# Optimization experiments

Measured on AMD Instinct MI355X. Metric: run time of the kernel, lower is better.

The kernel has to match this reference:

```python
import jax, jax.numpy as jnp
import numpy as np

CH = (16, 32, 16)
T_STEPS = 30
THRESH = 1.0


def conv3d(x, w, b):
    # x: (B, Cin, D, H, W), w: (Cout, Cin, kD, kH, kW), stride 2, VALID
    y = jax.lax.conv_general_dilated(
        x, w, window_strides=(2, 2, 2), padding='VALID',
        dimension_numbers=('NCDHW', 'OIDHW', 'NCDHW'))
    return y + b[None, :, None, None, None]


def setup_inputs() -> dict:
    key = jax.random.key(0)
    ks = jax.random.split(key, 11)
    B = 4
    x = jax.random.normal(ks[0], (B, 24, 602, 602), jnp.float32)

    def uinit(k, shape, fan_in):
        bound = 1.0 / np.sqrt(fan_in)
        return jax.random.uniform(k, shape, jnp.float32, -bound, bound)

    fan1 = 1 * 3 * 15 * 15
    fan2 = CH[0] * 3 * 15 * 15
    fan3 = CH[1] * 3 * 15 * 15
    w1 = uinit(ks[1], (CH[0], 1, 3, 15, 15), fan1)
    b1 = uinit(ks[2], (CH[0],), fan1)
    w2 = uinit(ks[3], (CH[1], CH[0], 3, 15, 15), fan2)
    b2 = uinit(ks[4], (CH[1],), fan2)
    w3 = uinit(ks[5], (CH[2], CH[1], 3, 15, 15), fan3)
    b3 = uinit(ks[6], (CH[2],), fan3)
    F1 = 21632 * CH[2] // 16  # 21632 for CH[2]=16
    fc1_w = uinit(ks[7], (512, F1), F1)
    fc1_b = uinit(ks[8], (512,), F1)
    fc2_w = uinit(ks[9], (54, 512), 512)
    fc2_b = uinit(ks[10], (54,), 512)
    return dict(x=x, w1=w1, b1=b1, w2=w2, b2=b2, w3=w3, b3=b3,
                fc1_w=fc1_w, fc1_b=fc1_b, fc2_w=fc2_w, fc2_b=fc2_b)


def _forward(x, w1, b1, w2, b2, w3, b3, fc1_w, fc1_b, fc2_w, fc2_b):
    B = x.shape[0]
    # avg_pool2d(kernel=2): (B,24,602,602) -> (B,24,301,301)
    xp = x.reshape(B, 24, 301, 2, 301, 2).mean(axis=(3, 5))
    h = xp[:, None]  # (B,1,24,301,301)
    h = jax.nn.relu(conv3d(h, w1, b1))  # (B,16,11,144,144)
    h = jax.nn.relu(conv3d(h, w2, b2))  # (B,32,5,65,65)
    h = jax.nn.relu(conv3d(h, w3, b3))  # (B,16,2,26,26)
    x_snn = h.reshape(B, -1)            # (B, 21632)

    sgn = jnp.sign(x_snn)
    prob = jnp.abs(x_snn) * 0.5

    def step(carry, k):
        m0, m1 = carry
        r = jax.random.uniform(k, x_snn.shape, x_snn.dtype)
        # Poisson encoding with straight-through gradient to x_snn
        spikes = (prob > r).astype(x_snn.dtype) * sgn
        p_in = jax.lax.stop_gradient(spikes - x_snn) + x_snn
        m0 = m0 + p_in @ fc1_w.T + fc1_b
        # LIF: threshold, subtract, spike with surrogate (pass-through where fired)
        fire = m0 > THRESH
        ex = jnp.where(fire, m0, 0.0)
        m0 = m0 - ex
        out = jnp.where(fire, ex - jax.lax.stop_gradient(ex) + 1.0, 0.0)
        m1 = m1 + out @ fc2_w.T + fc2_b
        return (m0, m1), None

    keys = jax.random.split(jax.random.key(42), T_STEPS)
    init = (jnp.zeros((B, 512), x_snn.dtype), jnp.zeros((B, 54), x_snn.dtype))
    (_, m1), _ = jax.lax.scan(step, init, keys)
    return m1


def reference(x, w1, b1, w2, b2, w3, b3, fc1_w, fc1_b, fc2_w, fc2_b):
    return _forward(x, w1, b1, w2, b2, w3, b3, fc1_w, fc1_b, fc2_w, fc2_b)
```

## Files before the change

### kernel.cpp

```cpp
#include <hip/hip_runtime.h>
#include <stdint.h>

struct SnnKeys { unsigned int k0[30]; unsigned int k1[30]; };

__host__ __device__ static inline void tf2x32(unsigned int k0, unsigned int k1,
                                              unsigned int& x0, unsigned int& x1) {
  unsigned int ks2 = k0 ^ k1 ^ 0x1BD11BDAu;
#define TF_RND(r) { x0 += x1; x1 = (x1 << (r)) | (x1 >> (32 - (r))); x1 ^= x0; }
  x0 += k0; x1 += k1;
  TF_RND(13) TF_RND(15) TF_RND(26) TF_RND(6)
  x0 += k1; x1 += ks2 + 1u;
  TF_RND(17) TF_RND(29) TF_RND(16) TF_RND(24)
  x0 += ks2; x1 += k0 + 2u;
  TF_RND(13) TF_RND(15) TF_RND(26) TF_RND(6)
  x0 += k0; x1 += k1 + 3u;
  TF_RND(17) TF_RND(29) TF_RND(16) TF_RND(24)
  x0 += k1; x1 += ks2 + 4u;
  TF_RND(13) TF_RND(15) TF_RND(26) TF_RND(6)
  x0 += ks2; x1 += k0 + 5u;
#undef TF_RND
}

#define POOL_N (4 * 24 * 301 * 301)

__global__ __launch_bounds__(256) void k_pool(const float* __restrict__ x,
                                              float* __restrict__ xp) {
  int i = blockIdx.x * 256 + threadIdx.x;
  if (i >= POOL_N) return;
  int j = i % 301;
  int rest = i / 301;
  int r = rest % 301;
  int bc = rest / 301;
  const float* src = x + ((size_t)bc * 602 + 2 * r) * 602 + 2 * j;
  float2 a = *(const float2*)src;
  float2 b = *(const float2*)(src + 602);
  xp[i] = 0.25f * ((a.x + a.y) + (b.x + b.y));
}

__global__ __launch_bounds__(256) void k_wt2(const float* __restrict__ w2,
                                             float* __restrict__ w2t) {
  int i = blockIdx.x * 256 + threadIdx.x;
  if (i >= 345600) return;
  int co = i & 31;
  int rest = i >> 5;
  int ci = rest / 675;
  int k675 = rest - ci * 675;
  w2t[i] = w2[((size_t)co * 16 + ci) * 675 + k675];
}

__global__ __launch_bounds__(256) void k_wt3(const float* __restrict__ w3,
                                             float* __restrict__ w3t) {
  int i = blockIdx.x * 256 + threadIdx.x;
  if (i >= 345600) return;
  int co = i & 15;
  int rest = i >> 4;
  int ci = rest / 675;
  int k675 = rest - ci * 675;
  w3t[i] = w3[((size_t)co * 32 + ci) * 675 + k675];
}

__global__ __launch_bounds__(256) void k_conv1(const float* __restrict__ xp,
                                               const float* __restrict__ w1,
                                               const float* __restrict__ b1,
                                               float* __restrict__ h1) {
  __shared__ alignas(16) float in_e[25 * 152];
  __shared__ alignas(16) float in_o[25 * 152];
  const int tid = threadIdx.x;
  const int wave = __builtin_amdgcn_readfirstlane(tid >> 6);
  const int lane = tid & 63;
  const int cog = wave >> 1, sg = wave & 1;
  const int cob = cog * 8;
  const int bz = blockIdx.y;
  const int b = bz / 11, d = bz % 11;
  const int s0 = blockIdx.x * 512;
  const int y0 = s0 / 144;

  int sq[4], be[4];
  bool vq[4];
#pragma unroll
  for (int q = 0; q < 4; ++q) {
    int s = s0 + sg * 256 + q * 64 + lane;
    vq[q] = (s < 20736);
    int sc = vq[q] ? s : 20735;
    int y = sc / 144, xx = sc - y * 144;
    sq[q] = s;
    be[q] = 2 * (y - y0) * 152 + xx;
  }

  float acc[8][4] = {};

  for (int kd = 0; kd < 3; ++kd) {
    __syncthreads();
    const int din = 2 * d + kd;
    const float* src = xp + (size_t)(b * 24 + din) * 90601;
    for (int i = tid; i < 25 * 301; i += 256) {
      int r = i / 301, c = i - r * 301;
      int gr = 2 * y0 + r;
      float v = (gr < 301) ? src[gr * 301 + c] : 0.0f;
      ((c & 1) ? in_o : in_e)[r * 152 + (c >> 1)] = v;
    }
    __syncthreads();
    const float* wp = w1 + cob * 675 + kd * 225;
    for (int kh = 0; kh < 15; ++kh) {
      float e[4][8], o[4][7];
#pragma unroll
      for (int q = 0; q < 4; ++q) {
        const float* pe = in_e + be[q] + kh * 152;
        const float* po = in_o + be[q] + kh * 152;
#pragma unroll
        for (int j = 0; j < 8; ++j) e[q][j] = pe[j];
#pragma unroll
        for (int j = 0; j < 7; ++j) o[q][j] = po[j];
      }
      const float* wk = wp + kh * 15;
#pragma unroll
      for (int j = 0; j < 8; ++j) {
#pragma unroll
        for (int c = 0; c < 8; ++c) {
          float wv = wk[c * 675 + 2 * j];
#pragma unroll
          for (int q = 0; q < 4; ++q) acc[c][q] += wv * e[q][j];
        }
      }
#pragma unroll
      for (int j = 0; j < 7; ++j) {
#pragma unroll
        for (int c = 0; c < 8; ++c) {
          float wv = wk[c * 675 + 2 * j + 1];
#pragma unroll
          for (int q = 0; q < 4; ++q) acc[c][q] += wv * o[q][j];
        }
      }
    }
  }
#pragma unroll
  for (int q = 0; q < 4; ++q) {
    if (vq[q]) {
#pragma unroll
      for (int c = 0; c < 8; ++c) {
        float v = acc[c][q] + b1[cob + c];
        h1[((size_t)(b * 16 + cob + c) * 11 + d) * 20736 + sq[q]] = fmaxf(v, 0.0f);
      }
    }
  }
}

__global__ __launch_bounds__(256) void k_conv2(const float* __restrict__ h1,
                                               const float* __restrict__ w2t,
                                               float* __restrict__ h2p) {
  __shared__ alignas(16) float in_e[23 * 72];
  __shared__ alignas(16) float in_o[23 * 72];
  const int tid = threadIdx.x;
  const int wave = __builtin_amdgcn_readfirstlane(tid >> 6);
  const int lane = tid & 63;
  const int cob = wave * 8;
  const int bz = blockIdx.y;
  const int cig = bz & 1;
  const int t5 = bz >> 1;
  const int b = t5 / 5, d = t5 % 5;
  const int s0 = blockIdx.x * 256;
  const int y0 = s0 / 65;

  int sq[4], be[4];
  bool vq[4];
#pragma unroll
  for (int q = 0; q < 4; ++q) {
    int s = s0 + q * 64 + lane;
    vq[q] = (s < 4225);
    int sc = vq[q] ? s : 4224;
    int y = sc / 65, xx = sc - y * 65;
    sq[q] = s;
    be[q] = 2 * (y - y0) * 72 + xx;
  }

  float acc[8][4] = {};

  for (int cil = 0; cil < 8; ++cil) {
    const int ci = cig * 8 + cil;
    for (int kd = 0; kd < 3; ++kd) {
      __syncthreads();
      const int din = 2 * d + kd;
      const float* src = h1 + (size_t)((b * 16 + ci) * 11 + din) * 20736;
      for (int i = tid; i < 23 * 36; i += 256) {
        int r = i / 36, c4 = i - r * 36;
        int gr = 2 * y0 + r;
        float4 v = {0.0f, 0.0f, 0.0f, 0.0f};
        if (gr < 144) v = *(const float4*)(src + gr * 144 + c4 * 4);
        *(float2*)&in_e[r * 72 + 2 * c4] = make_float2(v.x, v.z);
        *(float2*)&in_o[r * 72 + 2 * c4] = make_float2(v.y, v.w);
      }
      __syncthreads();
      const float* wkbase = w2t + (size_t)(ci * 3 + kd) * 225 * 32 + cob;
      for (int kh = 0; kh < 15; ++kh) {
        float e[4][8], o[4][7];
#pragma unroll
        for (int q = 0; q < 4; ++q) {
          const float* pe = in_e + be[q] + kh * 72;
          const float* po = in_o + be[q] + kh * 72;
#pragma unroll
          for (int j = 0; j < 8; ++j) e[q][j] = pe[j];
#pragma unroll
          for (int j = 0; j < 7; ++j) o[q][j] = po[j];
        }
        const float* wr = wkbase + kh * 15 * 32;
#pragma unroll
        for (int j = 0; j < 8; ++j) {
#pragma unroll
          for (int c = 0; c < 8; ++c) {
            float wv = wr[(2 * j) * 32 + c];
#pragma unroll
            for (int q = 0; q < 4; ++q) acc[c][q] += wv * e[q][j];
          }
        }
#pragma unroll
        for (int j = 0; j < 7; ++j) {
#pragma unroll
          for (int c = 0; c < 8; ++c) {
            float wv = wr[(2 * j + 1) * 32 + c];
#pragma unroll
            for (int q = 0; q < 4; ++q) acc[c][q] += wv * o[q][j];
          }
        }
      }
    }
  }
#pragma unroll
  for (int q = 0; q < 4; ++q) {
    if (vq[q]) {
#pragma unroll
      for (int c = 0; c < 8; ++c) {
        h2p[(size_t)cig * 2704000 +
            ((size_t)(b * 32 + cob + c) * 5 + d) * 4225 + sq[q]] = acc[c][q];
      }
    }
  }
}

__global__ __launch_bounds__(256) void k_h2fix(const float* __restrict__ p,
                                               const float* __restrict__ b2,
                                               float* __restrict__ h2) {
  int i = blockIdx.x * 256 + threadIdx.x;
  if (i >= 2704000) return;
  int co = (i / 21125) & 31;
  float v = p[i] + p[2704000 + i] + b2[co];
  h2[i] = fmaxf(v, 0.0f);
}

__global__ __launch_bounds__(256) void k_conv3(const float* __restrict__ h2,
                                               const float* __restrict__ w3t,
                                               float* __restrict__ h3p) {
  __shared__ alignas(16) float in_e[55 * 36];
  __shared__ alignas(16) float in_o[55 * 36];
  const int tid = threadIdx.x;
  const int wave = __builtin_amdgcn_readfirstlane(tid >> 6);
  const int lane = tid & 63;
  const int cog = wave >> 1, sg = wave & 1;
  const int cob = cog * 8;
  const int bz = blockIdx.y;
  const int b = bz >> 1, d = bz & 1;
  const int cig = blockIdx.z;
  const int s0 = blockIdx.x * 512;
  const int y0 = s0 / 26;

  int sq[4], be[4];
  bool vq[4];
#pragma unroll
  for (int q = 0; q < 4; ++q) {
    int s = s0 + sg * 256 + q * 64 + lane;
    vq[q] = (s < 676);
    int sc = vq[q] ? s : 675;
    int y = sc / 26, xx = sc - y * 26;
    sq[q] = s;
    be[q] = 2 * (y - y0) * 36 + xx;
  }

  float acc[8][4] = {};

  for (int cil = 0; cil < 2; ++cil) {
    const int ci = cig * 2 + cil;
    for (int kd = 0; kd < 3; ++kd) {
      __syncthreads();
      const int din = 2 * d + kd;
      const float* src = h2 + (size_t)((b * 32 + ci) * 5 + din) * 4225;
      for (int i = tid; i < 55 * 65; i += 256) {
        int r = i / 65, c = i - r * 65;
        int gr = 2 * y0 + r;
        float v = (gr < 65) ? src[gr * 65 + c] : 0.0f;
        ((c & 1) ? in_o : in_e)[r * 36 + (c >> 1)] = v;
      }
      __syncthreads();
      const float* wkbase = w3t + (size_t)(ci * 3 + kd) * 225 * 16 + cob;
      for (int kh = 0; kh < 15; ++kh) {
        float e[4][8], o[4][7];
#pragma unroll
        for (int q = 0; q < 4; ++q) {
          const float* pe = in_e + be[q] + kh * 36;
          const float* po = in_o + be[q] + kh * 36;
#pragma unroll
          for (int j = 0; j < 8; ++j) e[q][j] = pe[j];
#pragma unroll
          for (int j = 0; j < 7; ++j) o[q][j] = po[j];
        }
        const float* wr = wkbase + kh * 15 * 16;
#pragma unroll
        for (int j = 0; j < 8; ++j) {
#pragma unroll
          for (int c = 0; c < 8; ++c) {
            float wv = wr[(2 * j) * 16 + c];
#pragma unroll
            for (int q = 0; q < 4; ++q) acc[c][q] += wv * e[q][j];
          }
        }
#pragma unroll
        for (int j = 0; j < 7; ++j) {
#pragma unroll
          for (int c = 0; c < 8; ++c) {
            float wv = wr[(2 * j + 1) * 16 + c];
#pragma unroll
            for (int q = 0; q < 4; ++q) acc[c][q] += wv * o[q][j];
          }
        }
      }
    }
  }
#pragma unroll
  for (int q = 0; q < 4; ++q) {
    if (vq[q]) {
#pragma unroll
      for (int c = 0; c < 8; ++c) {
        h3p[(size_t)cig * 86528 +
            ((size_t)(b * 16 + cob + c) * 2 + d) * 676 + sq[q]] = acc[c][q];
      }
    }
  }
}

__global__ __launch_bounds__(256) void k_h3fix(const float* __restrict__ h3p,
                                               const float* __restrict__ b3,
                                               float* __restrict__ prob) {
  int p = blockIdx.x * 256 + threadIdx.x;
  if (p >= 86528) return;
  int co = (p % 21632) / 1352;
  float x = b3[co];
  for (int g = 0; g < 16; ++g) x += h3p[(size_t)g * 86528 + p];
  prob[p] = 0.5f * fmaxf(x, 0.0f);
}

__global__ __launch_bounds__(256) void k_spike(const float* __restrict__ prob,
                                               float* __restrict__ spk,
                                               SnnKeys keys) {
  int p = blockIdx.x * 256 + threadIdx.x;
  int t = blockIdx.y;
  float pr = prob[p];
  unsigned int x0 = 0u, x1 = (unsigned int)p;
  tf2x32(keys.k0[t], keys.k1[t], x0, x1);
  unsigned int bits = x0 ^ x1;
  float r = __uint_as_float((bits >> 9) | 0x3f800000u) - 1.0f;
  spk[(size_t)t * 86528 + p] = (pr > r) ? 1.0f : 0.0f;
}

__global__ __launch_bounds__(128) void k_fc1(const float* __restrict__ spk,
                                             const float* __restrict__ fc1w,
                                             float* __restrict__ incp) {
  __shared__ alignas(16) float slds[16][128];
  __shared__ alignas(16) float wlds[16][32];
  const int tx = threadIdx.x;
  const int ty = threadIdx.y;
  const int tid = ty * 8 + tx;
  const int nt = blockIdx.x;
  const int kc = blockIdx.y;
  const int k0base = kc * 1664;

  float acc[8][4];
#pragma unroll
  for (int mi = 0; mi < 8; ++mi)
#pragma unroll
    for (int ni = 0; ni < 4; ++ni) acc[mi][ni] = 0.0f;

  for (int kb = 0; kb < 1664; kb += 16) {
    const int k0 = k0base + kb;
    __syncthreads();
    {
      int m = tid;
      float4 v[4] = {{0,0,0,0},{0,0,0,0},{0,0,0,0},{0,0,0,0}};
      if (m < 120) {
        const float4* s = (const float4*)(spk + (size_t)m * 21632 + k0);
        v[0] = s[0]; v[1] = s[1]; v[2] = s[2]; v[3] = s[3];
      }
#pragma unroll
      for (int q = 0; q < 4; ++q) {
        slds[4 * q + 0][m] = v[q].x;
        slds[4 * q + 1][m] = v[q].y;
        slds[4 * q + 2][m] = v[q].z;
        slds[4 * q + 3][m] = v[q].w;
      }
    }
    for (int e = tid; e < 512; e += 128) {
      int n = e >> 4, kk = e & 15;
      wlds[kk][n] = fc1w[(size_t)(nt * 32 + n) * 21632 + k0 + kk];
    }
    __syncthreads();
#pragma unroll
    for (int kk = 0; kk < 16; ++kk) {
      const float4 wv = *(const float4*)&wlds[kk][tx * 4];
      const float4 s0 = *(const float4*)&slds[kk][ty * 8];
      const float4 s1 = *(const float4*)&slds[kk][ty * 8 + 4];
      float sv[8] = {s0.x, s0.y, s0.z, s0.w, s1.x, s1.y, s1.z, s1.w};
      float wz[4] = {wv.x, wv.y, wv.z, wv.w};
#pragma unroll
      for (int mi = 0; mi < 8; ++mi)
#pragma unroll
        for (int ni = 0; ni < 4; ++ni) acc[mi][ni] += sv[mi] * wz[ni];
    }
  }
#pragma unroll
  for (int mi = 0; mi < 8; ++mi) {
    int m = ty * 8 + mi;
    if (m < 120) {
      float4 o = {acc[mi][0], acc[mi][1], acc[mi][2], acc[mi][3]};
      *(float4*)&incp[((size_t)kc * 120 + m) * 512 + nt * 32 + tx * 4] = o;
    }
  }
}

__global__ __launch_bounds__(256) void k_scan(const float* __restrict__ incp,
                                              const float* __restrict__ fc1b,
                                              float* __restrict__ cnt) {
  int i = blockIdx.x * 256 + threadIdx.x;
  int b = i >> 9, n = i & 511;
  float bias = fc1b[n];
  float m0 = 0.0f, c = 0.0f;
  for (int t = 0; t < 30; ++t) {
    int m = t * 4 + b;
    float s = bias;
    for (int kc = 0; kc < 13; ++kc) s += incp[((size_t)kc * 120 + m) * 512 + n];
    m0 += s;
    if (m0 > 1.0f) { c += 1.0f; m0 = 0.0f; }
  }
  cnt[i] = c;
}

__global__ __launch_bounds__(256) void k_final(const float* __restrict__ cnt,
                                               const float* __restrict__ fc2w,
                                               const float* __restrict__ fc2b,
                                               float* __restrict__ out) {
  int o = threadIdx.x;
  if (o >= 216) return;
  int b = o / 54, oo = o - b * 54;
  const float* w = fc2w + (size_t)oo * 512;
  const float* c = cnt + (size_t)b * 512;
  float s = 0.0f;
  for (int n = 0; n < 512; ++n) s += c[n] * w[n];
  out[o] = s + 30.0f * fc2b[oo];
}

extern "C" void kernel_launch(void* const* d_in, const int* in_sizes, int n_in,
                              void* d_out, int out_size, void* d_ws, size_t ws_size,
                              hipStream_t stream) {
  (void)in_sizes; (void)n_in; (void)out_size; (void)ws_size;
  const float* x    = (const float*)d_in[0];
  const float* w1   = (const float*)d_in[1];
  const float* b1   = (const float*)d_in[2];
  const float* w2   = (const float*)d_in[3];
  const float* b2   = (const float*)d_in[4];
  const float* w3   = (const float*)d_in[5];
  const float* b3   = (const float*)d_in[6];
  const float* fc1w = (const float*)d_in[7];
  const float* fc1b = (const float*)d_in[8];
  const float* fc2w = (const float*)d_in[9];
  const float* fc2b = (const float*)d_in[10];
  float* out = (float*)d_out;
  float* ws  = (float*)d_ws;

  float* xp   = ws;
  float* h1   = ws + 8697696;
  float* w2t  = ws + 8112000;
  float* h2p  = ws;
  float* h2   = ws + 5408000;
  float* w3t  = ws;
  float* h3p  = ws + 8697696;
  float* prob = h3p + 16 * 86528;
  float* spk  = prob + 86528;
  float* incp = spk + 2595840;
  float* cnt  = incp + 13 * 61440;

  SnnKeys keys;
  for (int t = 0; t < 30; ++t) {
    unsigned int a = 0u, bb = (unsigned int)t;
    tf2x32(0u, 42u, a, bb);
    keys.k0[t] = a; keys.k1[t] = bb;
  }

  k_pool <<<(POOL_N + 255) / 256, 256, 0, stream>>>(x, xp);
  k_conv1<<<dim3(41, 44),    256, 0, stream>>>(xp, w1, b1, h1);
  k_wt2  <<<1350, 256, 0, stream>>>(w2, w2t);
  k_conv2<<<dim3(17, 40),    256, 0, stream>>>(h1, w2t, h2p);
  k_h2fix<<<(2704000 + 255) / 256, 256, 0, stream>>>(h2p, b2, h2);
  k_wt3  <<<1350, 256, 0, stream>>>(w3, w3t);
  k_conv3<<<dim3(2, 8, 16),  256, 0, stream>>>(h2, w3t, h3p);
  k_h3fix<<<338, 256, 0, stream>>>(h3p, b3, prob);
  k_spike<<<dim3(338, 30),   256, 0, stream>>>(prob, spk, keys);
  k_fc1  <<<dim3(16, 13), dim3(8, 16), 0, stream>>>(spk, fc1w, incp);
  k_scan <<<8, 256, 0, stream>>>(incp, fc1b, cnt);
  k_final<<<1, 256, 0, stream>>>(cnt, fc2w, fc2b, out);
}
```

Measured before the change: 1.903 ms.

## Retile conv kernels so each wave covers all 16 output channels

Conv1 now uses a transposed copy of w1 held in a device global, so channel weights sit contiguously. Each wave computes all 16 output channels for 3 spatial strips instead of 8 channels for 4. Conv2 moves to 16 channels by 2 strips per wave. Conv3 splits work per input channel over a full 65-row tile, giving 32 partial sums for h3fix to reduce. The aim is to reuse each loaded input value across more channels and cut redundant shared-memory reads, in exchange for more accumulator registers, which may lower occupancy, and more partial-sum traffic.

```diff
diff --git a/kernel.cpp b/kernel.cpp
--- a/kernel.cpp
+++ b/kernel.cpp
@@ -21,6 +21,8 @@
 #undef TF_RND
 }
 
+__device__ float g_w1t[10800];
+
 #define POOL_N (4 * 24 * 301 * 301)
 
 __global__ __launch_bounds__(256) void k_pool(const float* __restrict__ x,
@@ -37,6 +39,13 @@
   xp[i] = 0.25f * ((a.x + a.y) + (b.x + b.y));
 }
 
+__global__ __launch_bounds__(256) void k_wt1(const float* __restrict__ w1) {
+  int i = blockIdx.x * 256 + threadIdx.x;
+  if (i >= 10800) return;
+  int co = i & 15, k = i >> 4;
+  g_w1t[i] = w1[(size_t)co * 675 + k];
+}
+
 __global__ __launch_bounds__(256) void k_wt2(const float* __restrict__ w2,
                                              float* __restrict__ w2t) {
   int i = blockIdx.x * 256 + threadIdx.x;
@@ -60,26 +69,22 @@
 }
 
 __global__ __launch_bounds__(256) void k_conv1(const float* __restrict__ xp,
-                                               const float* __restrict__ w1,
                                                const float* __restrict__ b1,
                                                float* __restrict__ h1) {
   __shared__ alignas(16) float in_e[25 * 152];
   __shared__ alignas(16) float in_o[25 * 152];
   const int tid = threadIdx.x;
-  const int wave = __builtin_amdgcn_readfirstlane(tid >> 6);
-  const int lane = tid & 63;
-  const int cog = wave >> 1, sg = wave & 1;
-  const int cob = cog * 8;
+  const int wave = tid >> 6, lane = tid & 63;
   const int bz = blockIdx.y;
   const int b = bz / 11, d = bz % 11;
-  const int s0 = blockIdx.x * 512;
+  const int s0 = blockIdx.x * 768;
   const int y0 = s0 / 144;
 
-  int sq[4], be[4];
-  bool vq[4];
-#pragma unroll
-  for (int q = 0; q < 4; ++q) {
-    int s = s0 + sg * 256 + q * 64 + lane;
+  int sq[3], be[3];
+  bool vq[3];
+#pragma unroll
+  for (int q = 0; q < 3; ++q) {
+    int s = s0 + wave * 192 + q * 64 + lane;
     vq[q] = (s < 20736);
     int sc = vq[q] ? s : 20735;
     int y = sc / 144, xx = sc - y * 144;
@@ -87,7 +92,7 @@
     be[q] = 2 * (y - y0) * 152 + xx;
   }
 
-  float acc[8][4] = {};
+  float acc[16][3] = {};
 
   for (int kd = 0; kd < 3; ++kd) {
     __syncthreads();
@@ -100,11 +105,11 @@
       ((c & 1) ? in_o : in_e)[r * 152 + (c >> 1)] = v;
     }
     __syncthreads();
-    const float* wp = w1 + cob * 675 + kd * 225;
+    const float* wd = g_w1t + kd * 225 * 16;
     for (int kh = 0; kh < 15; ++kh) {
-      float e[4][8], o[4][7];
-#pragma unroll
-      for (int q = 0; q < 4; ++q) {
+      float e[3][8], o[3][7];
+#pragma unroll
+      for (int q = 0; q < 3; ++q) {
         const float* pe = in_e + be[q] + kh * 152;
         const float* po = in_o + be[q] + kh * 152;
 #pragma unroll
@@ -112,34 +117,34 @@
 #pragma unroll
         for (int j = 0; j < 7; ++j) o[q][j] = po[j];
       }
-      const float* wk = wp + kh * 15;
+      const float* wk = wd + kh * 15 * 16;
 #pragma unroll
       for (int j = 0; j < 8; ++j) {
 #pragma unroll
-        for (int c = 0; c < 8; ++c) {
-          float wv = wk[c * 675 + 2 * j];
-#pragma unroll
-          for (int q = 0; q < 4; ++q) acc[c][q] += wv * e[q][j];
+        for (int c = 0; c < 16; ++c) {
+          float wv = wk[(2 * j) * 16 + c];
+#pragma unroll
+          for (int q = 0; q < 3; ++q) acc[c][q] += wv * e[q][j];
         }
       }
 #pragma unroll
       for (int j = 0; j < 7; ++j) {
 #pragma unroll
-        for (int c = 0; c < 8; ++c) {
-          float wv = wk[c * 675 + 2 * j + 1];
-#pragma unroll
-          for (int q = 0; q < 4; ++q) acc[c][q] += wv * o[q][j];
-        }
-      }
-    }
-  }
-#pragma unroll
-  for (int q = 0; q < 4; ++q) {
+        for (int c = 0; c < 16; ++c) {
+          float wv = wk[(2 * j + 1) * 16 + c];
+#pragma unroll
+          for (int q = 0; q < 3; ++q) acc[c][q] += wv * o[q][j];
+        }
+      }
+    }
+  }
+#pragma unroll
+  for (int q = 0; q < 3; ++q) {
     if (vq[q]) {
 #pragma unroll
-      for (int c = 0; c < 8; ++c) {
-        float v = acc[c][q] + b1[cob + c];
-        h1[((size_t)(b * 16 + cob + c) * 11 + d) * 20736 + sq[q]] = fmaxf(v, 0.0f);
+      for (int c = 0; c < 16; ++c) {
+        float v = acc[c][q] + b1[c];
+        h1[((size_t)(b * 16 + c) * 11 + d) * 20736 + sq[q]] = fmaxf(v, 0.0f);
       }
     }
   }
@@ -151,9 +156,9 @@
   __shared__ alignas(16) float in_e[23 * 72];
   __shared__ alignas(16) float in_o[23 * 72];
   const int tid = threadIdx.x;
-  const int wave = __builtin_amdgcn_readfirstlane(tid >> 6);
-  const int lane = tid & 63;
-  const int cob = wave * 8;
+  const int wave = tid >> 6, lane = tid & 63;
+  const int cob = (wave & 1) * 16;
+  const int sg = wave >> 1;
   const int bz = blockIdx.y;
   const int cig = bz & 1;
   const int t5 = bz >> 1;
@@ -161,11 +166,11 @@
   const int s0 = blockIdx.x * 256;
   const int y0 = s0 / 65;
 
-  int sq[4], be[4];
-  bool vq[4];
-#pragma unroll
-  for (int q = 0; q < 4; ++q) {
-    int s = s0 + q * 64 + lane;
+  int sq[2], be[2];
+  bool vq[2];
+#pragma unroll
+  for (int q = 0; q < 2; ++q) {
+    int s = s0 + sg * 128 + q * 64 + lane;
     vq[q] = (s < 4225);
     int sc = vq[q] ? s : 4224;
     int y = sc / 65, xx = sc - y * 65;
@@ -173,7 +178,7 @@
     be[q] = 2 * (y - y0) * 72 + xx;
   }
 
-  float acc[8][4] = {};
+  float acc[16][2] = {};
 
   for (int cil = 0; cil < 8; ++cil) {
     const int ci = cig * 8 + cil;
@@ -190,11 +195,11 @@
         *(float2*)&in_o[r * 72 + 2 * c4] = make_float2(v.y, v.w);
       }
       __syncthreads();
-      const float* wkbase = w2t + (size_t)(ci * 3 + kd) * 225 * 32 + cob;
+      const float* wdk = w2t + (size_t)(ci * 3 + kd) * 7200 + cob;
       for (int kh = 0; kh < 15; ++kh) {
-        float e[4][8], o[4][7];
-#pragma unroll
-        for (int q = 0; q < 4; ++q) {
+        float e[2][8], o[2][7];
+#pragma unroll
+        for (int q = 0; q < 2; ++q) {
           const float* pe = in_e + be[q] + kh * 72;
           const float* po = in_o + be[q] + kh * 72;
 #pragma unroll
@@ -202,33 +207,33 @@
 #pragma unroll
           for (int j = 0; j < 7; ++j) o[q][j] = po[j];
         }
-        const float* wr = wkbase + kh * 15 * 32;
+        const float* wk = wdk + kh * 15 * 32;
 #pragma unroll
         for (int j = 0; j < 8; ++j) {
 #pragma unroll
-          for (int c = 0; c < 8; ++c) {
-            float wv = wr[(2 * j) * 32 + c];
-#pragma unroll
-            for (int q = 0; q < 4; ++q) acc[c][q] += wv * e[q][j];
+          for (int c = 0; c < 16; ++c) {
+            float wv = wk[(2 * j) * 32 + c];
+#pragma unroll
+            for (int q = 0; q < 2; ++q) acc[c][q] += wv * e[q][j];
           }
         }
 #pragma unroll
         for (int j = 0; j < 7; ++j) {
 #pragma unroll
-          for (int c = 0; c < 8; ++c) {
-            float wv = wr[(2 * j + 1) * 32 + c];
-#pragma unroll
-            for (int q = 0; q < 4; ++q) acc[c][q] += wv * o[q][j];
+          for (int c = 0; c < 16; ++c) {
+            float wv = wk[(2 * j + 1) * 32 + c];
+#pragma unroll
+            for (int q = 0; q < 2; ++q) acc[c][q] += wv * o[q][j];
           }
         }
       }
     }
   }
 #pragma unroll
-  for (int q = 0; q < 4; ++q) {
+  for (int q = 0; q < 2; ++q) {
     if (vq[q]) {
 #pragma unroll
-      for (int c = 0; c < 8; ++c) {
+      for (int c = 0; c < 16; ++c) {
         h2p[(size_t)cig * 2704000 +
             ((size_t)(b * 32 + cob + c) * 5 + d) * 4225 + sq[q]] = acc[c][q];
       }
@@ -249,87 +254,78 @@
 __global__ __launch_bounds__(256) void k_conv3(const float* __restrict__ h2,
                                                const float* __restrict__ w3t,
                                                float* __restrict__ h3p) {
-  __shared__ alignas(16) float in_e[55 * 36];
-  __shared__ alignas(16) float in_o[55 * 36];
+  __shared__ alignas(16) float in_e[65 * 36];
+  __shared__ alignas(16) float in_o[65 * 36];
   const int tid = threadIdx.x;
-  const int wave = __builtin_amdgcn_readfirstlane(tid >> 6);
-  const int lane = tid & 63;
-  const int cog = wave >> 1, sg = wave & 1;
-  const int cob = cog * 8;
-  const int bz = blockIdx.y;
-  const int b = bz >> 1, d = bz & 1;
-  const int cig = blockIdx.z;
-  const int s0 = blockIdx.x * 512;
-  const int y0 = s0 / 26;
-
-  int sq[4], be[4];
-  bool vq[4];
-#pragma unroll
-  for (int q = 0; q < 4; ++q) {
-    int s = s0 + sg * 256 + q * 64 + lane;
+  const int wave = tid >> 6, lane = tid & 63;
+  const int bx = blockIdx.x;
+  const int b = bx >> 1, d = bx & 1;
+  const int ci = blockIdx.y;
+
+  int sq[3], be[3];
+  bool vq[3];
+#pragma unroll
+  for (int q = 0; q < 3; ++q) {
+    int s = wave * 192 + q * 64 + lane;
     vq[q] = (s < 676);
     int sc = vq[q] ? s : 675;
     int y = sc / 26, xx = sc - y * 26;
     sq[q] = s;
-    be[q] = 2 * (y - y0) * 36 + xx;
-  }
-
-  float acc[8][4] = {};
-
-  for (int cil = 0; cil < 2; ++cil) {
-    const int ci = cig * 2 + cil;
-    for (int kd = 0; kd < 3; ++kd) {
-      __syncthreads();
-      const int din = 2 * d + kd;
-      const float* src = h2 + (size_t)((b * 32 + ci) * 5 + din) * 4225;
-      for (int i = tid; i < 55 * 65; i += 256) {
-        int r = i / 65, c = i - r * 65;
-        int gr = 2 * y0 + r;
-        float v = (gr < 65) ? src[gr * 65 + c] : 0.0f;
-        ((c & 1) ? in_o : in_e)[r * 36 + (c >> 1)] = v;
-      }
-      __syncthreads();
-      const float* wkbase = w3t + (size_t)(ci * 3 + kd) * 225 * 16 + cob;
-      for (int kh = 0; kh < 15; ++kh) {
-        float e[4][8], o[4][7];
-#pragma unroll
-        for (int q = 0; q < 4; ++q) {
-          const float* pe = in_e + be[q] + kh * 36;
-          const float* po = in_o + be[q] + kh * 36;
-#pragma unroll
-          for (int j = 0; j < 8; ++j) e[q][j] = pe[j];
-#pragma unroll
-          for (int j = 0; j < 7; ++j) o[q][j] = po[j];
-        }
-        const float* wr = wkbase + kh * 15 * 16;
-#pragma unroll
-        for (int j = 0; j < 8; ++j) {
-#pragma unroll
-          for (int c = 0; c < 8; ++c) {
-            float wv = wr[(2 * j) * 16 + c];
-#pragma unroll
-            for (int q = 0; q < 4; ++q) acc[c][q] += wv * e[q][j];
-          }
-        }
-#pragma unroll
-        for (int j = 0; j < 7; ++j) {
-#pragma unroll
-          for (int c = 0; c < 8; ++c) {
-            float wv = wr[(2 * j + 1) * 16 + c];
-#pragma unroll
-            for (int q = 0; q < 4; ++q) acc[c][q] += wv * o[q][j];
-          }
-        }
-      }
-    }
-  }
-#pragma unroll
-  for (int q = 0; q < 4; ++q) {
+    be[q] = 2 * y * 36 + xx;
+  }
+
+  float acc[16][3] = {};
+
+  for (int kd = 0; kd < 3; ++kd) {
+    __syncthreads();
+    const int din = 2 * d + kd;
+    const float* src = h2 + (size_t)((b * 32 + ci) * 5 + din) * 4225;
+    for (int i = tid; i < 4225; i += 256) {
+      int r = i / 65, c = i - r * 65;
+      float v = src[i];
+      ((c & 1) ? in_o : in_e)[r * 36 + (c >> 1)] = v;
+    }
+    __syncthreads();
+    const float* wdk = w3t + (size_t)(ci * 3 + kd) * 3600;
+    for (int kh = 0; kh < 15; ++kh) {
+      float e[3][8], o[3][7];
+#pragma unroll
+      for (int q = 0; q < 3; ++q) {
+        const float* pe = in_e + be[q] + kh * 36;
+        const float* po = in_o + be[q] + kh * 36;
+#pragma unroll
+        for (int j = 0; j < 8; ++j) e[q][j] = pe[j];
+#pragma unroll
+        for (int j = 0; j < 7; ++j) o[q][j] = po[j];
+      }
+      const float* wk = wdk + kh * 15 * 16;
+#pragma unroll
+      for (int j = 0; j < 8; ++j) {
+#pragma unroll
+        for (int c = 0; c < 16; ++c) {
+          float wv = wk[(2 * j) * 16 + c];
+#pragma unroll
+          for (int q = 0; q < 3; ++q) acc[c][q] += wv * e[q][j];
+        }
+      }
+#pragma unroll
+      for (int j = 0; j < 7; ++j) {
+#pragma unroll
+        for (int c = 0; c < 16; ++c) {
+          float wv = wk[(2 * j + 1) * 16 + c];
+#pragma unroll
+          for (int q = 0; q < 3; ++q) acc[c][q] += wv * o[q][j];
+        }
+      }
+    }
+  }
+#pragma unroll
+  for (int q = 0; q < 3; ++q) {
     if (vq[q]) {
 #pragma unroll
-      for (int c = 0; c < 8; ++c) {
-        h3p[(size_t)cig * 86528 +
-            ((size_t)(b * 16 + cob + c) * 2 + d) * 676 + sq[q]] = acc[c][q];
+      for (int c = 0; c < 16; ++c) {
+        h3p[(size_t)ci * 86528 +
+            ((size_t)(b * 16 + c) * 2 + d) * 676 + sq[q]] = acc[c][q];
       }
     }
   }
@@ -342,7 +338,7 @@
   if (p >= 86528) return;
   int co = (p % 21632) / 1352;
   float x = b3[co];
-  for (int g = 0; g < 16; ++g) x += h3p[(size_t)g * 86528 + p];
+  for (int g = 0; g < 32; ++g) x += h3p[(size_t)g * 86528 + p];
   prob[p] = 0.5f * fmaxf(x, 0.0f);
 }
 
@@ -479,7 +475,7 @@
   float* h2   = ws + 5408000;
   float* w3t  = ws;
   float* h3p  = ws + 8697696;
-  float* prob = h3p + 16 * 86528;
+  float* prob = h3p + 32 * 86528;
   float* spk  = prob + 86528;
   float* incp = spk + 2595840;
   float* cnt  = incp + 13 * 61440;
@@ -492,12 +488,13 @@
   }
 
   k_pool <<<(POOL_N + 255) / 256, 256, 0, stream>>>(x, xp);
-  k_conv1<<<dim3(41, 44),    256, 0, stream>>>(xp, w1, b1, h1);
+  k_wt1  <<<43, 256, 0, stream>>>(w1);
+  k_conv1<<<dim3(27, 44),    256, 0, stream>>>(xp, b1, h1);
   k_wt2  <<<1350, 256, 0, stream>>>(w2, w2t);
   k_conv2<<<dim3(17, 40),    256, 0, stream>>>(h1, w2t, h2p);
   k_h2fix<<<(2704000 + 255) / 256, 256, 0, stream>>>(h2p, b2, h2);
   k_wt3  <<<1350, 256, 0, stream>>>(w3, w3t);
-  k_conv3<<<dim3(2, 8, 16),  256, 0, stream>>>(h2, w3t, h3p);
+  k_conv3<<<dim3(8, 32),     256, 0, stream>>>(h2, w3t, h3p);
   k_h3fix<<<338, 256, 0, stream>>>(h3p, b3, prob);
   k_spike<<<dim3(338, 30),   256, 0, stream>>>(prob, spk, keys);
   k_fc1  <<<dim3(16, 13), dim3(8, 16), 0, stream>>>(spk, fc1w, incp);
```

Result: slower. 2.778 ms (+46.0%).
